# Optimization experiments

Hardware: AMD Instinct MI355X
Metric: run time of the kernel (lower is better)

Reference implementation:

```python
import jax, jax.numpy as jnp
import numpy as np

N, E, F_IN, HID, HEADS, NCLS, NG = 50000, 800000, 128, 128, 4, 10, 512
C = HID // HEADS          # per-head channels
BN_EPS = 1e-5
NEG_SLOPE = 0.2           # SuperGATConv default negative_slope
N_CONV = 3


def setup_inputs() -> dict:
    key = jax.random.key(0)
    ks = jax.random.split(key, 16)
    x = jax.random.normal(ks[0], (N, F_IN), jnp.float32)
    # edges with no self loops (reference appends self loops itself, as SuperGATConv does)
    src = jax.random.randint(ks[1], (E,), 0, N, dtype=jnp.int32)
    off = jax.random.randint(ks[2], (E,), 1, N, dtype=jnp.int32)
    dst = (src + off) % N
    edge_index = jnp.stack([src, dst], axis=0)
    batch = jnp.sort(jax.random.randint(ks[3], (N,), 0, NG, dtype=jnp.int32))
    s = 0.1
    # BatchNorm params per module init: weight=1, bias=1e-4 (running stats fresh: mean=0, var=1)
    inp = {
        "x": x, "edge_index": edge_index, "batch": batch,
        "bn_feat_g": jnp.ones((F_IN,), jnp.float32), "bn_feat_b": jnp.full((F_IN,), 1e-4, jnp.float32),
        "w_feat": jax.random.normal(ks[4], (F_IN, HID), jnp.float32) * s,
        "b_feat": jnp.zeros((HID,), jnp.float32),
        "bn_conv_g": jnp.ones((N_CONV, HID), jnp.float32), "bn_conv_b": jnp.full((N_CONV, HID), 1e-4, jnp.float32),
        "w_gat": jax.random.normal(ks[5], (N_CONV, HID, HID), jnp.float32) * s,
        "att_l": jax.random.normal(ks[6], (N_CONV, HEADS, C), jnp.float32) * s,
        "att_r": jax.random.normal(ks[7], (N_CONV, HEADS, C), jnp.float32) * s,
        "b_gat": jnp.zeros((N_CONV, HID), jnp.float32),
        "bn_fc_g": jnp.ones((HID,), jnp.float32), "bn_fc_b": jnp.full((HID,), 1e-4, jnp.float32),
        "w_fc": jax.random.normal(ks[8], (HID, HID), jnp.float32) * s,
        "b_fc": jnp.zeros((HID,), jnp.float32),
        "bn_hid_g": jnp.ones((HID,), jnp.float32), "bn_hid_b": jnp.full((HID,), 1e-4, jnp.float32),
        "w_cls": jax.random.normal(ks[9], (HID, NCLS), jnp.float32) * s,
        "b_cls": jnp.zeros((NCLS,), jnp.float32),
    }
    return inp


def _bn_eval(h, g, b):
    # eval-mode BatchNorm1d with fresh running stats (mean=0, var=1)
    return h * (g / jnp.sqrt(1.0 + BN_EPS)) + b


def _segment_softmax(a, seg, num_segments):
    # softmax over edges grouped by destination node (PyG softmax semantics)
    m = jax.ops.segment_max(a, seg, num_segments=num_segments)
    a = jnp.exp(a - m[seg])
    s = jax.ops.segment_sum(a, seg, num_segments=num_segments)
    return a / (s[seg] + 1e-16)


def _supergat_mx(h, src, dst, W, att_l, att_r, bias):
    # h: [N, HID] -> per-head features [N, H, C]
    hh = (h @ W).reshape(N, HEADS, C)
    h_j = hh[src]  # source (message) features  [E2, H, C]
    h_i = hh[dst]  # destination features       [E2, H, C]
    logits = jnp.einsum('ehc,ehc->eh', h_i, h_j)                       # MX dot-product
    alpha = jnp.einsum('ehc,hc->eh', h_j, att_l) + jnp.einsum('ehc,hc->eh', h_i, att_r)
    alpha = alpha * jax.nn.sigmoid(logits)
    alpha = jax.nn.leaky_relu(alpha, NEG_SLOPE)
    alpha = _segment_softmax(alpha, dst, N)                            # [E2, H]
    out = jax.ops.segment_sum(h_j * alpha[..., None], dst, num_segments=N)
    return out.reshape(N, HID) + bias


def reference(x, edge_index, batch, bn_feat_g, bn_feat_b, w_feat, b_feat,
              bn_conv_g, bn_conv_b, w_gat, att_l, att_r, b_gat,
              bn_fc_g, bn_fc_b, w_fc, b_fc, bn_hid_g, bn_hid_b, w_cls, b_cls):
    loops = jnp.arange(N, dtype=edge_index.dtype)
    src = jnp.concatenate([edge_index[0], loops])   # SuperGATConv adds self loops
    dst = jnp.concatenate([edge_index[1], loops])
    h = _bn_eval(x, bn_feat_g, bn_feat_b)
    h = jax.nn.relu(h @ w_feat + b_feat)            # GCNConv(gfn=True) == Linear
    for i in range(N_CONV):
        h = _bn_eval(h, bn_conv_g[i], bn_conv_b[i])
        h = jax.nn.relu(_supergat_mx(h, src, dst, w_gat[i], att_l[i], att_r[i], b_gat[i]))
    g = jax.ops.segment_sum(h, batch, num_segments=NG)  # global_add_pool -> [NG, HID]
    g = _bn_eval(g, bn_fc_g, bn_fc_b)
    g = jax.nn.relu(g @ w_fc + b_fc)
    g = _bn_eval(g, bn_hid_g, bn_hid_b)
    logits = g @ w_cls + b_cls
    att_loss = jnp.float32(0.0)  # eval mode: no edge-sampled attention loss
    return jax.nn.log_softmax(logits, axis=-1), att_loss
```

## Files before the change

### kernel.cpp

```cpp
#include <hip/hip_runtime.h>

#define NN 50000
#define EE 800000
#define FHID 128
#define NHEAD 4
#define NGRAPH 512
#define NCLS 10
#define BK 256
#define BCH 2048
#define NBLK_E 391
#define NBUCK 196
#define CAPB 6144

typedef unsigned short u16;
typedef unsigned int u32;
typedef unsigned long long u64;
typedef __attribute__((ext_vector_type(8))) short bf16x8;
typedef __attribute__((ext_vector_type(4))) float f32x4;

__device__ __forceinline__ float bf2f(u16 u){
    union { u32 i; float f; } v; v.i = ((u32)u) << 16; return v.f;
}
__device__ __forceinline__ float bflo(u32 u){
    union { u32 i; float f; } v; v.i = u << 16; return v.f;
}
__device__ __forceinline__ float bfhi(u32 u){
    union { u32 i; float f; } v; v.i = u & 0xffff0000u; return v.f;
}
__device__ __forceinline__ u16 f2bf(float f){
    union { float f; u32 i; } v; v.f = f;
    u32 r = v.i + 0x7fffu + ((v.i >> 16) & 1u);
    return (u16)(r >> 16);
}
__device__ __forceinline__ u32 pack2(float a, float b){
    return ((u32)f2bf(b) << 16) | f2bf(a);
}
__device__ __forceinline__ float loadF(const void* p, int i, int isf32){
    return isf32 ? ((const float*)p)[i] : bf2f(((const u16*)p)[i]);
}
__device__ __forceinline__ void unpk8(uint4 v, float* f){
    f[0]=bflo(v.x); f[1]=bfhi(v.x);
    f[2]=bflo(v.y); f[3]=bfhi(v.y);
    f[4]=bflo(v.z); f[5]=bfhi(v.z);
    f[6]=bflo(v.w); f[7]=bfhi(v.w);
}

__device__ __forceinline__ float quad_red(float x){
    int t0 = __builtin_amdgcn_mov_dpp(__float_as_int(x), 0xB1, 0xF, 0xF, true);
    float y = x + __int_as_float(t0);
    int t1 = __builtin_amdgcn_mov_dpp(__float_as_int(y), 0x4E, 0xF, 0xF, true);
    return y + __int_as_float(t1);
}

__device__ int detect_local(const u16* x, int tid, int nthreads, int* lds){
    int ok = 0;
    for (int i = tid; i < 1024; i += nthreads){
        u16 u = x[i];
        int e = (u >> 7) & 0xFF;
        if ((u & 0x7fff) == 0 || (e >= 0x70 && e <= 0x85)) ok++;
    }
    lds[tid] = ok;
    __syncthreads();
    for (int o2 = nthreads >> 1; o2 > 0; o2 >>= 1){
        if (tid < o2) lds[tid] += lds[tid + o2];
        __syncthreads();
    }
    int r = (lds[0] < 900) ? 1 : 0;
    __syncthreads();
    return r;
}

__global__ __launch_bounds__(256) void prep_all(
        const u16* __restrict__ xz,
        const void* w_feat, const void* b_feat, const void* bn_feat_g, const void* bn_feat_b,
        const void* w_gat, const void* bn_conv_g, const void* bn_conv_b, const void* b_gat,
        const void* wfc, const void* bfc, const void* bnfg, const void* bnfb,
        const void* bnhg, const void* bnhb, const void* wcls, const void* bcls,
        const void* attl, const void* attr,
        u16* __restrict__ Wt, float* __restrict__ cvec, float* __restrict__ biasv,
        float* __restrict__ hp, int* __restrict__ dflag, int* __restrict__ gcur)
{
    __shared__ int ldsi[256];
    __shared__ float red[128];
    int bid = blockIdx.x, t = threadIdx.x;
    int isf32 = detect_local(xz, t, 256, ldsi);
    if (bid == 0){
        if (t == 0) dflag[0] = isf32;
        gcur[t] = t * CAPB;
    }

    if (bid < 512){
        if (t >= 128) return;
        int L = bid >> 7;
        int n = bid & 127;
        int k = t;
        const float rs = rsqrtf(1.0f + 1e-5f);
        float wv, bg, bb;
        if (L == 0){
            wv = loadF(w_feat, k*FHID + n, isf32);
            bg = loadF(bn_feat_g, k, isf32);
            bb = loadF(bn_feat_b, k, isf32);
        } else {
            wv = loadF(w_gat, (L-1)*FHID*FHID + k*FHID + n, isf32);
            bg = loadF(bn_conv_g, (L-1)*FHID + k, isf32);
            bb = loadF(bn_conv_b, (L-1)*FHID + k, isf32);
        }
        Wt[L*FHID*FHID + n*FHID + k] = f2bf(bg * rs * wv);
        red[k] = bb * wv;
        __syncthreads();
        for (int o2 = 64; o2 > 0; o2 >>= 1){
            if (k < o2) red[k] += red[k + o2];
            __syncthreads();
        }
        if (k == 0){
            float c = red[0];
            if (L == 0) c += loadF(b_feat, n, isf32);
            cvec[L*FHID + n] = c;
            if (L > 0) biasv[L*FHID + n] = loadF(b_gat, (L-1)*FHID + n, isf32);
        }
    } else {
        int gt = (bid - 512)*256 + t;
        for (int i = gt; i < FHID*FHID; i += 16*256) hp[i] = loadF(wfc, i, isf32);
        if (gt < FHID*NCLS) hp[16384 + gt] = loadF(wcls, gt, isf32);
        if (gt >= 2048 && gt < 2048 + 3*FHID){
            int i = gt - 2048;
            hp[18320 + i] = loadF(attl, i, isf32);
            hp[18704 + i] = loadF(attr, i, isf32);
        }
        if (gt >= 2560 && gt < 2560 + FHID){
            int tt = gt - 2560;
            hp[17664 + tt] = loadF(bnfg, tt, isf32);
            hp[17792 + tt] = loadF(bnfb, tt, isf32);
            hp[17920 + tt] = loadF(bfc,  tt, isf32);
            hp[18048 + tt] = loadF(bnhg, tt, isf32);
            hp[18176 + tt] = loadF(bnhb, tt, isf32);
        }
        if (gt >= 3072 && gt < 3072 + NCLS) hp[18304 + (gt - 3072)] = loadF(bcls, gt - 3072, isf32);
    }
}

__global__ __launch_bounds__(256) void gemm128(const void* __restrict__ A,
                                               const u16* __restrict__ Wt,
                                               const float* __restrict__ cvec,
                                               u16* __restrict__ out, int relu,
                                               int araw, const int* __restrict__ flag,
                                               const float* __restrict__ attl,
                                               const float* __restrict__ attr,
                                               float* __restrict__ al,
                                               float* __restrict__ ar)
{
    int wave = threadIdx.x >> 6;
    int lane = threadIdx.x & 63;
    int m = lane & 15, quad = lane >> 4;
    int row = blockIdx.x * 64 + wave * 16 + m;
    bool v0 = row < NN;
    bool f32in = araw && flag[0];
    const u16*  Au = (const u16*)A;
    const float* Af = (const float*)A;
    f32x4 acc[8];
#pragma unroll
    for (int j = 0; j < 8; j++) acc[j] = (f32x4){0.f,0.f,0.f,0.f};
#pragma unroll
    for (int t = 0; t < 4; t++){
        bf16x8 a0 = {0,0,0,0,0,0,0,0};
        int kof = t*32 + quad*8;
        if (f32in){
            if (v0){
                const float* p = Af + (size_t)row*FHID + kof;
                float4 u0 = *(const float4*)p, u1 = *(const float4*)(p+4);
                a0[0]=(short)f2bf(u0.x); a0[1]=(short)f2bf(u0.y);
                a0[2]=(short)f2bf(u0.z); a0[3]=(short)f2bf(u0.w);
                a0[4]=(short)f2bf(u1.x); a0[5]=(short)f2bf(u1.y);
                a0[6]=(short)f2bf(u1.z); a0[7]=(short)f2bf(u1.w);
            }
        } else {
            if (v0) a0 = *(const bf16x8*)(Au + (size_t)row*FHID + kof);
        }
#pragma unroll
        for (int ct = 0; ct < 8; ct++){
            bf16x8 wfrag = *(const bf16x8*)(Wt + (ct*16 + m)*FHID + kof);
            acc[ct] = __builtin_amdgcn_mfma_f32_16x16x32_bf16(wfrag, a0, acc[ct], 0, 0, 0);
        }
    }
    bool doa = (attl != nullptr);
    float sl[4] = {0.f,0.f,0.f,0.f};
    float sr[4] = {0.f,0.f,0.f,0.f};
#pragma unroll
    for (int ct = 0; ct < 8; ct++){
        int cb = ct*16 + quad*4;
        float4 cv = *(const float4*)(cvec + cb);
        float w0 = acc[ct][0] + cv.x;
        float w1 = acc[ct][1] + cv.y;
        float w2 = acc[ct][2] + cv.z;
        float w3 = acc[ct][3] + cv.w;
        if (relu){
            w0 = fmaxf(w0, 0.f); w1 = fmaxf(w1, 0.f);
            w2 = fmaxf(w2, 0.f); w3 = fmaxf(w3, 0.f);
        }
        if (doa){
            int h = ct >> 1;
            float4 tl = *(const float4*)(attl + cb);
            float4 tr = *(const float4*)(attr + cb);
            sl[h] += w0*tl.x + w1*tl.y + w2*tl.z + w3*tl.w;
            sr[h] += w0*tr.x + w1*tr.y + w2*tr.z + w3*tr.w;
        }
        if (v0){
            uint2 st; st.x = pack2(w0, w1); st.y = pack2(w2, w3);
            *(uint2*)(out + (size_t)row*FHID + cb) = st;
        }
    }
    if (doa){
#pragma unroll
        for (int h = 0; h < 4; h++){
            sl[h] += __shfl_xor(sl[h], 16, 64);
            sl[h] += __shfl_xor(sl[h], 32, 64);
            sr[h] += __shfl_xor(sr[h], 16, 64);
            sr[h] += __shfl_xor(sr[h], 32, 64);
        }
        if (v0){
            al[row*NHEAD + quad] = sl[quad];
            ar[row*NHEAD + quad] = sr[quad];
        }
    }
}

__global__ __launch_bounds__(256) void bin_edges(const int* __restrict__ srcp,
        const int* __restrict__ dstp, int* __restrict__ gcur, u64* __restrict__ binned)
{
    __shared__ int h[BK], lb[BK], gb[BK], cur[BK];
    __shared__ u64 stage[BCH];
    int t = threadIdx.x;
    h[t] = 0;
    __syncthreads();
    int base = blockIdx.x * BCH;
    int sv[8], dv[8];
#pragma unroll
    for (int k = 0; k < 8; k++){
        int e = base + k*256 + t;
        int d = -1, s = 0;
        if (e < EE){
            d = dstp[e]; s = srcp[e];
            if ((u32)d >= NN) d = -1;
        }
        sv[k] = s; dv[k] = d;
        if (d >= 0) atomicAdd(&h[d >> 8], 1);
    }
    __syncthreads();
    lb[t] = h[t];
    __syncthreads();
    for (int off = 1; off < BK; off <<= 1){
        int x = (t >= off) ? lb[t - off] : 0;
        __syncthreads();
        lb[t] += x;
        __syncthreads();
    }
    int excl = lb[t] - h[t];
    int tot  = lb[BK-1];
    __syncthreads();
    lb[t] = excl;
    gb[t] = h[t] ? atomicAdd(&gcur[t], h[t]) : 0;
    cur[t] = 0;
    __syncthreads();
#pragma unroll
    for (int k = 0; k < 8; k++){
        int d = dv[k];
        if (d >= 0){
            int b = d >> 8;
            int p = lb[b] + atomicAdd(&cur[b], 1);
            stage[p] = ((u64)(u32)d << 32) | (u32)sv[k];
        }
    }
    __syncthreads();
    for (int i = t; i < tot; i += 256){
        u64 pr = stage[i];
        int b = (int)(pr >> 40);
        binned[gb[b] + (i - lb[b])] = pr;
    }
}

__global__ __launch_bounds__(512) void build_csr(const u64* __restrict__ binned,
        const int* __restrict__ gcur, int2* __restrict__ rowdeg, int* __restrict__ colbuf)
{
    __shared__ int deg[BK], ls[BK], cur[BK];
    __shared__ int colstage[CAPB];
    int b = blockIdx.x, t = threadIdx.x;
    int gb = b * CAPB;
    int cnt = gcur[b] - gb;
    if (cnt < 0) cnt = 0;
    if (cnt > CAPB) cnt = CAPB;
    if (t < BK) deg[t] = 0;
    __syncthreads();
    for (int i = t; i < cnt; i += 512){
        int d = (int)(binned[gb + i] >> 32);
        atomicAdd(&deg[d & 255], 1);
    }
    __syncthreads();
    if (t < BK) ls[t] = deg[t];
    __syncthreads();
    for (int off = 1; off < BK; off <<= 1){
        int x = (t < BK && t >= off) ? ls[t - off] : 0;
        __syncthreads();
        if (t < BK) ls[t] += x;
        __syncthreads();
    }
    if (t < BK){
        int excl = ls[t] - deg[t];
        int node = b*256 + t;
        if (node < NN) rowdeg[node] = (int2){gb + excl, gb + excl + deg[t]};
        cur[t] = excl;
    }
    __syncthreads();
    for (int i = t; i < cnt; i += 512){
        u64 pr = binned[gb + i];
        int d = (int)(pr >> 32) & 255;
        int s = (int)(u32)pr;
        int p = atomicAdd(&cur[d], 1);
        colstage[p] = s;
    }
    __syncthreads();
    for (int i = t; i < cnt; i += 512) colbuf[gb + i] = colstage[i];
}

struct EdgeGrp {
    uint4 x0, x1, x2, x3;
    float f0, f1, f2, f3;
};

__device__ __forceinline__ void load_grp(EdgeGrp& G, const int* __restrict__ colbuf,
        int g, const u16* __restrict__ hh, const float* __restrict__ al,
        int chbase, int head)
{
    int i0 = colbuf[g+0], i1 = colbuf[g+1], i2 = colbuf[g+2], i3 = colbuf[g+3];
    if ((u32)i0 >= NN) i0 = 0;
    if ((u32)i1 >= NN) i1 = 0;
    if ((u32)i2 >= NN) i2 = 0;
    if ((u32)i3 >= NN) i3 = 0;
    G.x0 = *(const uint4*)(hh + (size_t)i0*FHID + chbase);
    G.x1 = *(const uint4*)(hh + (size_t)i1*FHID + chbase);
    G.x2 = *(const uint4*)(hh + (size_t)i2*FHID + chbase);
    G.x3 = *(const uint4*)(hh + (size_t)i3*FHID + chbase);
    G.f0 = al[i0*NHEAD + head];
    G.f1 = al[i1*NHEAD + head];
    G.f2 = al[i2*NHEAD + head];
    G.f3 = al[i3*NHEAD + head];
}

__device__ __forceinline__ void comp_edge(uint4 xv, float af, bool ev,
        const float* hd, float arn, float& s, float* o)
{
    float hs[8]; unpk8(xv, hs);
    float lg = hd[0]*hs[0]+hd[1]*hs[1]+hd[2]*hs[2]+hd[3]*hs[3]
             + hd[4]*hs[4]+hd[5]*hs[5]+hd[6]*hs[6]+hd[7]*hs[7];
    lg = quad_red(lg);
    float a2 = (af + arn) * (1.0f / (1.0f + __expf(-lg)));
    a2 = (a2 > 0.0f) ? a2 : 0.2f*a2;
    float pe = __expf(fminf(a2, 60.f));
    if (!ev) pe = 0.f;
    s += pe;
#pragma unroll
    for (int i = 0; i < 8; i++) o[i] += pe*hs[i];
}

__device__ __forceinline__ void comp_grp(const EdgeGrp& G, int g, int e1,
        const float* hd, float arn, float& s, float* o)
{
    comp_edge(G.x0, G.f0, g+0 < e1, hd, arn, s, o);
    comp_edge(G.x1, G.f1, g+1 < e1, hd, arn, s, o);
    comp_edge(G.x2, G.f2, g+2 < e1, hd, arn, s, o);
    comp_edge(G.x3, G.f3, g+3 < e1, hd, arn, s, o);
}

__global__ __launch_bounds__(256) void supergat_conv(const u16* __restrict__ hh,
        const float* __restrict__ al, const float* __restrict__ ar,
        const int2* __restrict__ rowdeg, const int* __restrict__ colbuf,
        const float* __restrict__ bias, u16* __restrict__ hout)
{
    int wid  = (blockIdx.x*256 + threadIdx.x) >> 6;
    int lane = threadIdx.x & 63;
    int group = lane >> 4;
    int gl    = lane & 15;
    int head  = gl >> 2;
    int q     = gl & 3;
    int node  = wid*4 + group;
    bool valid = node < NN;
    int snode = valid ? node : 0;
    int chbase = head*32 + q*8;

    uint4 hdv = *(const uint4*)(hh + (size_t)snode*FHID + chbase);
    float hd[8]; unpk8(hdv, hd);
    float arn = ar[snode*NHEAD + head];
    float aln = al[snode*NHEAD + head];

    float d = hd[0]*hd[0]+hd[1]*hd[1]+hd[2]*hd[2]+hd[3]*hd[3]
            + hd[4]*hd[4]+hd[5]*hd[5]+hd[6]*hd[6]+hd[7]*hd[7];
    d = quad_red(d);
    float a = (aln + arn) * (1.0f / (1.0f + __expf(-d)));
    a = (a > 0.0f) ? a : 0.2f*a;
    float p = __expf(fminf(a, 60.f));
    float s = p;
    float o[8];
#pragma unroll
    for (int i = 0; i < 8; i++) o[i] = p*hd[i];

    int2 rd = valid ? rowdeg[node] : (int2){0,0};
    int e0 = rd.x, e1 = rd.y;
    if (e0 < 0) e0 = 0;
    if (e1 > BK*CAPB) e1 = BK*CAPB;

    EdgeGrp A, B;
    int g = e0;
    if (g < e1){
        load_grp(A, colbuf, g, hh, al, chbase, head);
        while (true){
            int gn = g + 4;
            if (gn >= e1){ comp_grp(A, g, e1, hd, arn, s, o); break; }
            load_grp(B, colbuf, gn, hh, al, chbase, head);
            comp_grp(A, g, e1, hd, arn, s, o);
            g = gn; gn = g + 4;
            if (gn >= e1){ comp_grp(B, g, e1, hd, arn, s, o); break; }
            load_grp(A, colbuf, gn, hh, al, chbase, head);
            comp_grp(B, g, e1, hd, arn, s, o);
            g = gn;
        }
    }

    if (valid){
        float inv = 1.0f / (s + 1e-16f);
        uint4 w;
        w.x = pack2(fmaxf(o[0]*inv + bias[chbase+0], 0.f),
                    fmaxf(o[1]*inv + bias[chbase+1], 0.f));
        w.y = pack2(fmaxf(o[2]*inv + bias[chbase+2], 0.f),
                    fmaxf(o[3]*inv + bias[chbase+3], 0.f));
        w.z = pack2(fmaxf(o[4]*inv + bias[chbase+4], 0.f),
                    fmaxf(o[5]*inv + bias[chbase+5], 0.f));
        w.w = pack2(fmaxf(o[6]*inv + bias[chbase+6], 0.f),
                    fmaxf(o[7]*inv + bias[chbase+7], 0.f));
        *(uint4*)(hout + (size_t)node*FHID + chbase) = w;
    }
}

__global__ void pool_head(const u16* __restrict__ h, const int* __restrict__ batch,
                          const float* __restrict__ hp, const int* __restrict__ flag,
                          void* __restrict__ out)
{
    __shared__ int bounds[2];
    __shared__ float gb[FHID];
    __shared__ float g2[FHID];
    __shared__ float lg[16];
    int gi = blockIdx.x, t = threadIdx.x;
    int isf32 = flag[0];
    if (t < 2){
        int target = gi + t;
        int lo = 0, hi = NN;
        while (lo < hi){
            int mid = (lo + hi) >> 1;
            if (batch[mid] < target) lo = mid + 1; else hi = mid;
        }
        bounds[t] = lo;
    }
    __syncthreads();
    float s0 = 0.f, s1 = 0.f, s2 = 0.f, s3 = 0.f;
    int node = bounds[0], nend = bounds[1];
    for (; node + 3 < nend; node += 4){
        s0 += bf2f(h[(size_t)(node+0)*FHID + t]);
        s1 += bf2f(h[(size_t)(node+1)*FHID + t]);
        s2 += bf2f(h[(size_t)(node+2)*FHID + t]);
        s3 += bf2f(h[(size_t)(node+3)*FHID + t]);
    }
    for (; node < nend; node++) s0 += bf2f(h[(size_t)node*FHID + t]);
    float acc0 = (s0 + s1) + (s2 + s3);
    const float rs = rsqrtf(1.0f + 1e-5f);
    gb[t] = acc0 * (hp[17664 + t] * rs) + hp[17792 + t];
    __syncthreads();
    float acc = hp[17920 + t];
    for (int k = 0; k < FHID; k++) acc += gb[k] * hp[k*FHID + t];
    acc = fmaxf(acc, 0.f);
    g2[t] = acc * (hp[18048 + t] * rs) + hp[18176 + t];
    __syncthreads();
    if (t < NCLS){
        float l = hp[18304 + t];
        for (int k = 0; k < FHID; k++) l += g2[k] * hp[16384 + k*NCLS + t];
        lg[t] = l;
    }
    __syncthreads();
    if (t == 0){
        float mx = lg[0];
        for (int j = 1; j < NCLS; j++) mx = fmaxf(mx, lg[j]);
        float se = 0.f;
        for (int j = 0; j < NCLS; j++) se += __expf(lg[j] - mx);
        float lse = logf(se) + mx;
        if (isf32){
            float* o = (float*)out;
            for (int j = 0; j < NCLS; j++) o[gi*NCLS + j] = lg[j] - lse;
            if (gi == 0) o[NGRAPH*NCLS] = 0.f;
        } else {
            u16* o = (u16*)out;
            for (int j = 0; j < NCLS; j++) o[gi*NCLS + j] = f2bf(lg[j] - lse);
            if (gi == 0) o[NGRAPH*NCLS] = 0;
        }
    }
}

extern "C" void kernel_launch(void* const* d_in, const int* in_sizes, int n_in,
                              void* d_out, int out_size, void* d_ws, size_t ws_size,
                              hipStream_t stream)
{
    (void)in_sizes; (void)n_in; (void)out_size; (void)ws_size;
    const void* x         = d_in[0];
    const int* edge       = (const int*)d_in[1];
    const int* batch      = (const int*)d_in[2];

    char* ws = (char*)d_ws;
    size_t off = 0;
    auto alloc = [&](size_t bytes) -> char* {
        char* p = ws + off; off += (bytes + 255) & ~(size_t)255; return p;
    };
    int*   dflag   = (int*)  alloc(256);
    u16*   WtAll   = (u16*)  alloc((size_t)4*FHID*FHID*2);
    float* cvecAll = (float*)alloc((size_t)4*FHID*4);
    float* biasv   = (float*)alloc((size_t)4*FHID*4);
    float* headp   = (float*)alloc((size_t)19088*4);
    float* al      = (float*)alloc((size_t)NN*NHEAD*4);
    float* ar      = (float*)alloc((size_t)NN*NHEAD*4);
    int*   gcur    = (int*)  alloc((size_t)BK*4);
    int2*  rowdeg  = (int2*) alloc((size_t)NN*8);
    int*   colbuf  = (int*)  alloc((size_t)(BK*CAPB + 16)*4);
    u16*   hA      = (u16*)  alloc((size_t)NN*FHID*2);
    u16*   hB      = (u16*)  alloc((size_t)NN*FHID*2);
    u64*   binned  = (u64*)hB;

    const int* srcp = edge;
    const int* dstp = edge + EE;

    prep_all<<<528, 256, 0, stream>>>((const u16*)x,
        d_in[5], d_in[6], d_in[3], d_in[4], d_in[9], d_in[7], d_in[8], d_in[12],
        d_in[15], d_in[16], d_in[13], d_in[14], d_in[17], d_in[18], d_in[19], d_in[20],
        d_in[10], d_in[11],
        WtAll, cvecAll, biasv, headp, dflag, gcur);

    bin_edges<<<NBLK_E, 256, 0, stream>>>(srcp, dstp, gcur, binned);
    build_csr<<<NBUCK, 512, 0, stream>>>(binned, gcur, rowdeg, colbuf);

    gemm128<<<(NN + 63)/64, 256, 0, stream>>>(x, WtAll, cvecAll, hA, 1, 1, dflag,
                                              nullptr, nullptr, nullptr, nullptr);

    for (int i = 0; i < 3; i++){
        gemm128<<<(NN + 63)/64, 256, 0, stream>>>(hA, WtAll + (i+1)*FHID*FHID,
                                                  cvecAll + (i+1)*FHID, hB, 0, 0, dflag,
                                                  headp + 18320 + i*FHID,
                                                  headp + 18704 + i*FHID, al, ar);
        supergat_conv<<<(NN + 15)/16, 256, 0, stream>>>(hB, al, ar, rowdeg, colbuf,
                                                        biasv + (i+1)*FHID, hA);
    }

    pool_head<<<NGRAPH, 128, 0, stream>>>(hA, batch, headp, dflag, d_out);
}
```

Before: 414.0 us.

## Assign one wavefront per node and split edges across four lane groups

```diff
diff --git a/kernel.cpp b/kernel.cpp
--- a/kernel.cpp
+++ b/kernel.cpp
@@ -321,75 +321,50 @@
     for (int i = t; i < cnt; i += 512) colbuf[gb + i] = colstage[i];
 }
 
-struct EdgeGrp {
-    uint4 x0, x1, x2, x3;
-    float f0, f1, f2, f3;
-};
-
-__device__ __forceinline__ void load_grp(EdgeGrp& G, const int* __restrict__ colbuf,
-        int g, const u16* __restrict__ hh, const float* __restrict__ al,
-        int chbase, int head)
-{
-    int i0 = colbuf[g+0], i1 = colbuf[g+1], i2 = colbuf[g+2], i3 = colbuf[g+3];
-    if ((u32)i0 >= NN) i0 = 0;
-    if ((u32)i1 >= NN) i1 = 0;
-    if ((u32)i2 >= NN) i2 = 0;
-    if ((u32)i3 >= NN) i3 = 0;
-    G.x0 = *(const uint4*)(hh + (size_t)i0*FHID + chbase);
-    G.x1 = *(const uint4*)(hh + (size_t)i1*FHID + chbase);
-    G.x2 = *(const uint4*)(hh + (size_t)i2*FHID + chbase);
-    G.x3 = *(const uint4*)(hh + (size_t)i3*FHID + chbase);
-    G.f0 = al[i0*NHEAD + head];
-    G.f1 = al[i1*NHEAD + head];
-    G.f2 = al[i2*NHEAD + head];
-    G.f3 = al[i3*NHEAD + head];
-}
-
-__device__ __forceinline__ void comp_edge(uint4 xv, float af, bool ev,
+__device__ __forceinline__ void load_e(uint4& X, float& F, bool& V, int& e, int e1,
+        const int* __restrict__ colbuf, const u16* __restrict__ hh,
+        const float* __restrict__ al, int chbase, int head)
+{
+    V = e < e1;
+    int si = colbuf[e];
+    if (!V || (u32)si >= NN) si = 0;
+    X = *(const uint4*)(hh + (size_t)si*FHID + chbase);
+    F = al[si*NHEAD + head];
+    e += 4;
+}
+
+__device__ __forceinline__ void comp_e(uint4 X, float F, bool V,
         const float* hd, float arn, float& s, float* o)
 {
-    float hs[8]; unpk8(xv, hs);
+    float hs[8]; unpk8(X, hs);
     float lg = hd[0]*hs[0]+hd[1]*hs[1]+hd[2]*hs[2]+hd[3]*hs[3]
              + hd[4]*hs[4]+hd[5]*hs[5]+hd[6]*hs[6]+hd[7]*hs[7];
     lg = quad_red(lg);
-    float a2 = (af + arn) * (1.0f / (1.0f + __expf(-lg)));
+    float a2 = (F + arn) * (1.0f / (1.0f + __expf(-lg)));
     a2 = (a2 > 0.0f) ? a2 : 0.2f*a2;
-    float pe = __expf(fminf(a2, 60.f));
-    if (!ev) pe = 0.f;
+    float pe = V ? __expf(fminf(a2, 60.f)) : 0.f;
     s += pe;
 #pragma unroll
     for (int i = 0; i < 8; i++) o[i] += pe*hs[i];
 }
 
-__device__ __forceinline__ void comp_grp(const EdgeGrp& G, int g, int e1,
-        const float* hd, float arn, float& s, float* o)
-{
-    comp_edge(G.x0, G.f0, g+0 < e1, hd, arn, s, o);
-    comp_edge(G.x1, G.f1, g+1 < e1, hd, arn, s, o);
-    comp_edge(G.x2, G.f2, g+2 < e1, hd, arn, s, o);
-    comp_edge(G.x3, G.f3, g+3 < e1, hd, arn, s, o);
-}
-
-__global__ __launch_bounds__(256) void supergat_conv(const u16* __restrict__ hh,
+__global__ __launch_bounds__(256, 8) void supergat_conv(const u16* __restrict__ hh,
         const float* __restrict__ al, const float* __restrict__ ar,
         const int2* __restrict__ rowdeg, const int* __restrict__ colbuf,
         const float* __restrict__ bias, u16* __restrict__ hout)
 {
-    int wid  = (blockIdx.x*256 + threadIdx.x) >> 6;
+    int node = (blockIdx.x*256 + threadIdx.x) >> 6;
     int lane = threadIdx.x & 63;
     int group = lane >> 4;
     int gl    = lane & 15;
     int head  = gl >> 2;
-    int q     = gl & 3;
-    int node  = wid*4 + group;
-    bool valid = node < NN;
-    int snode = valid ? node : 0;
-    int chbase = head*32 + q*8;
-
-    uint4 hdv = *(const uint4*)(hh + (size_t)snode*FHID + chbase);
+    int chbase = head*32 + (gl & 3)*8;
+    if (node >= NN) return;
+
+    uint4 hdv = *(const uint4*)(hh + (size_t)node*FHID + chbase);
     float hd[8]; unpk8(hdv, hd);
-    float arn = ar[snode*NHEAD + head];
-    float aln = al[snode*NHEAD + head];
+    float arn = ar[node*NHEAD + head];
+    float aln = al[node*NHEAD + head];
 
     float d = hd[0]*hd[0]+hd[1]*hd[1]+hd[2]*hd[2]+hd[3]*hd[3]
             + hd[4]*hd[4]+hd[5]*hd[5]+hd[6]*hd[6]+hd[7]*hd[7];
@@ -397,34 +372,43 @@
     float a = (aln + arn) * (1.0f / (1.0f + __expf(-d)));
     a = (a > 0.0f) ? a : 0.2f*a;
     float p = __expf(fminf(a, 60.f));
+    if (group != 0) p = 0.f;
     float s = p;
     float o[8];
 #pragma unroll
     for (int i = 0; i < 8; i++) o[i] = p*hd[i];
 
-    int2 rd = valid ? rowdeg[node] : (int2){0,0};
+    int2 rd = rowdeg[node];
     int e0 = rd.x, e1 = rd.y;
     if (e0 < 0) e0 = 0;
     if (e1 > BK*CAPB) e1 = BK*CAPB;
-
-    EdgeGrp A, B;
-    int g = e0;
-    if (g < e1){
-        load_grp(A, colbuf, g, hh, al, chbase, head);
+    int it = (e1 - e0 + 3) >> 2;
+    int e = e0 + group;
+
+    if (it > 0){
+        uint4 xA, xB; float fA, fB; bool vA, vB;
+        load_e(xA, fA, vA, e, e1, colbuf, hh, al, chbase, head);
         while (true){
-            int gn = g + 4;
-            if (gn >= e1){ comp_grp(A, g, e1, hd, arn, s, o); break; }
-            load_grp(B, colbuf, gn, hh, al, chbase, head);
-            comp_grp(A, g, e1, hd, arn, s, o);
-            g = gn; gn = g + 4;
-            if (gn >= e1){ comp_grp(B, g, e1, hd, arn, s, o); break; }
-            load_grp(A, colbuf, gn, hh, al, chbase, head);
-            comp_grp(B, g, e1, hd, arn, s, o);
-            g = gn;
-        }
-    }
-
-    if (valid){
+            if (it == 1){ comp_e(xA, fA, vA, hd, arn, s, o); break; }
+            load_e(xB, fB, vB, e, e1, colbuf, hh, al, chbase, head);
+            comp_e(xA, fA, vA, hd, arn, s, o);
+            --it;
+            if (it == 1){ comp_e(xB, fB, vB, hd, arn, s, o); break; }
+            load_e(xA, fA, vA, e, e1, colbuf, hh, al, chbase, head);
+            comp_e(xB, fB, vB, hd, arn, s, o);
+            --it;
+        }
+    }
+
+    s += __shfl_xor(s, 16, 64);
+    s += __shfl_xor(s, 32, 64);
+#pragma unroll
+    for (int i = 0; i < 8; i++){
+        o[i] += __shfl_xor(o[i], 16, 64);
+        o[i] += __shfl_xor(o[i], 32, 64);
+    }
+
+    if (group == 0){
         float inv = 1.0f / (s + 1e-16f);
         uint4 w;
         w.x = pack2(fmaxf(o[0]*inv + bias[chbase+0], 0.f),
@@ -549,8 +533,8 @@
                                                   cvecAll + (i+1)*FHID, hB, 0, 0, dflag,
                                                   headp + 18320 + i*FHID,
                                                   headp + 18704 + i*FHID, al, ar);
-        supergat_conv<<<(NN + 15)/16, 256, 0, stream>>>(hB, al, ar, rowdeg, colbuf,
-                                                        biasv + (i+1)*FHID, hA);
+        supergat_conv<<<(NN + 3)/4, 256, 0, stream>>>(hB, al, ar, rowdeg, colbuf,
+                                                      biasv + (i+1)*FHID, hA);
     }
 
     pool_head<<<NGRAPH, 128, 0, stream>>>(hA, batch, headp, dflag, d_out);
```

After: 378.2 us. 8.7% less time.
